# Optimization experiments

Hardware: AMD Instinct MI355X
Metric: run time of the kernel (lower is better)

Reference implementation:

```python
import jax, jax.numpy as jnp
import numpy as np

T, H, I, E, K = 2048, 2048, 1408, 8, 2


def setup_inputs() -> dict:
    key = jax.random.key(0)
    k1, k2, k3, k4, k5 = jax.random.split(key, 5)
    s_h = 1.0 / np.sqrt(H)
    s_i = 1.0 / np.sqrt(I)
    return {
        "hidden_states": jax.random.normal(k1, (T, H), dtype=jnp.float32),
        "router_logits": jax.random.normal(k2, (T, E), dtype=jnp.float32),
        "Wg": jax.random.normal(k3, (E, H, I), dtype=jnp.float32) * s_h,
        "Wu": jax.random.normal(k4, (E, H, I), dtype=jnp.float32) * s_h,
        "Wd": jax.random.normal(k5, (E, I, H), dtype=jnp.float32) * s_i,
        "top_k": K,
    }


def reference(hidden_states, router_logits, Wg, Wu, Wd, top_k):
    # top-k routing: softmax over the selected top-k logits (as in torch.topk + softmax)
    topk_vals, topk_ids = jax.lax.top_k(router_logits, top_k)  # [T,K]
    topk_w = jax.nn.softmax(topk_vals, axis=-1)                # [T,K]

    n_tok = hidden_states.shape[0]
    n_exp = router_logits.shape[-1]
    # combine weights [T,E]: scatter top-k weights back to expert slots
    cw = jnp.zeros((n_tok, n_exp), hidden_states.dtype)
    cw = cw.at[jnp.arange(n_tok)[:, None], topk_ids].add(topk_w)

    out = jnp.zeros_like(hidden_states)
    for e in range(n_exp):  # small fixed expert count
        g = hidden_states @ Wg[e]          # [T,I]
        u = hidden_states @ Wu[e]          # [T,I]
        y = (jax.nn.silu(g) * u) @ Wd[e]   # [T,H]
        out = out + cw[:, e:e + 1] * y
    return out
```

## Files before the change

### kernel.cpp

```cpp
#include <hip/hip_runtime.h>
#include <hip/hip_bf16.h>
#include <cstdint>
#include <cstddef>

#define TT 2048
#define HH 2048
#define II 1408
#define EE 8
#define MAXROWS 5120

typedef unsigned short u16;
typedef __attribute__((ext_vector_type(8))) __bf16 bf16x8;
typedef __attribute__((ext_vector_type(4))) float f32x4;

typedef const __attribute__((address_space(1))) uint32_t* gas1_t;
typedef __attribute__((address_space(3))) uint32_t* las3_t;

#define VM_WAIT(N) asm volatile("s_waitcnt vmcnt(" #N ")" ::: "memory")
#define IR_FENCE() asm volatile("" ::: "memory")

__device__ __forceinline__ float bf2f(u16 b) {
    return __uint_as_float(((uint32_t)b) << 16);
}
__device__ __forceinline__ u16 f2bf(float x) {
    uint32_t u = __float_as_uint(x);
    u += 0x7fffu + ((u >> 16) & 1u);
    return (u16)(u >> 16);
}

__global__ void k_sniff(const u16* __restrict__ raw, int* __restrict__ flag,
                        int* __restrict__ counts) {
    __shared__ int cnt;
    if (threadIdx.x < EE) counts[threadIdx.x] = 0;
    if (threadIdx.x == 0) cnt = 0;
    __syncthreads();
    int w = 0;
    for (int i = threadIdx.x; i < 4096; i += 256) {
        u16 x = raw[i];
        if (x & 0x7fff) {
            int ex = (x >> 7) & 0xff;
            if (ex == 0xff || ex < 100 || ex > 140) ++w;
        }
    }
    atomicAdd(&cnt, w);
    __syncthreads();
    if (threadIdx.x == 0) flag[0] = (cnt > 100) ? 1 : 0;
}

__global__ void k_routing2(const void* __restrict__ logits, const int* __restrict__ flag,
                           int* __restrict__ counts, int* __restrict__ idx,
                           float* __restrict__ wt, int* __restrict__ slot) {
    int t = blockIdx.x * 256 + threadIdx.x;
    if (t >= TT) return;
    const int f = flag[0];
    float v[EE];
#pragma unroll
    for (int e = 0; e < EE; ++e)
        v[e] = f ? ((const float*)logits)[t * EE + e]
                 : bf2f(((const u16*)logits)[t * EE + e]);
    int i0 = 0; float v0 = v[0];
#pragma unroll
    for (int e = 1; e < EE; ++e) { if (v[e] > v0) { v0 = v[e]; i0 = e; } }
    int i1 = -1; float v1 = -3.4e38f;
#pragma unroll
    for (int e = 0; e < EE; ++e) { if (e != i0 && v[e] > v1) { v1 = v[e]; i1 = e; } }
    float r = __expf(v1 - v0);
    float s = 1.f / (1.f + r);
    int p0 = atomicAdd(&counts[i0], 1);
    idx[i0 * TT + p0] = t; wt[i0 * TT + p0] = s;
    slot[t * 2 + 0] = i0 * TT + p0;
    int p1 = atomicAdd(&counts[i1], 1);
    idx[i1 * TT + p1] = t; wt[i1 * TT + p1] = r * s;
    slot[t * 2 + 1] = i1 * TT + p1;
}

__global__ void k_offsets(const int* __restrict__ counts, int* __restrict__ meta) {
    if (threadIdx.x == 0 && blockIdx.x == 0) {
        int off = 0;
        for (int e = 0; e < EE; ++e) {
            int c = counts[e];
            int p = (c + 127) & ~127;
            meta[e] = off; meta[8 + e] = p;
            off += p;
        }
    }
}

__global__ void k_cast(const void* __restrict__ src, const int* __restrict__ flag,
                       u16* __restrict__ dst) {
    const int i0 = (blockIdx.x * 256 + threadIdx.x) * 8;
    if (flag[0]) {
        const float* s = (const float*)src;
#pragma unroll
        for (int j = 0; j < 8; ++j) dst[i0 + j] = f2bf(s[i0 + j]);
    } else {
        const u16* s = (const u16*)src;
        *(uint4*)&dst[i0] = *(const uint4*)&s[i0];
    }
}

__global__ void k_transposeV(const void* __restrict__ src, const int* __restrict__ flag,
                             u16* __restrict__ dst, int R, int C) {
    __shared__ u16 t[64][68];
    const size_t eo = (size_t)blockIdx.z * (size_t)R * (size_t)C;
    const int r0 = blockIdx.y * 64, c0 = blockIdx.x * 64;
    const int tid = threadIdx.x;
    const int f = flag[0];
    {
        const int cg = tid & 15, rr = tid >> 4;
#pragma unroll
        for (int p = 0; p < 4; ++p) {
            const int r = rr + p * 16;
            const size_t base = eo + (size_t)(r0 + r) * C + c0 + cg * 4;
            if (f) {
                const float4 v = *(const float4*)((const float*)src + base);
                t[r][cg * 4 + 0] = f2bf(v.x); t[r][cg * 4 + 1] = f2bf(v.y);
                t[r][cg * 4 + 2] = f2bf(v.z); t[r][cg * 4 + 3] = f2bf(v.w);
            } else {
                const ushort4 v = *(const ushort4*)((const u16*)src + base);
                t[r][cg * 4 + 0] = v.x; t[r][cg * 4 + 1] = v.y;
                t[r][cg * 4 + 2] = v.z; t[r][cg * 4 + 3] = v.w;
            }
        }
    }
    __syncthreads();
    {
        const int rg = tid & 15, cc = tid >> 4;
#pragma unroll
        for (int p = 0; p < 4; ++p) {
            const int c = cc + p * 16;
            ushort4 o;
            o.x = t[rg * 4 + 0][c]; o.y = t[rg * 4 + 1][c];
            o.z = t[rg * 4 + 2][c]; o.w = t[rg * 4 + 3][c];
            *(ushort4*)(dst + eo + (size_t)(c0 + c) * R + r0 + rg * 4) = o;
        }
    }
}


#define G1_COMPUTE(B) do { \
    __builtin_amdgcn_s_setprio(1); \
    bf16x8 af[4]; \
    _Pragma("unroll") \
    for (int mi = 0; mi < 4; ++mi) \
        af[mi] = *(const bf16x8*)&As[B][(wr + mi * 16 + ln) * 32 + qx]; \
    _Pragma("unroll") \
    for (int ni = 0; ni < 2; ++ni) { \
        bf16x8 bgf = *(const bf16x8*)&Bg[B][(wc + ni * 16 + ln) * 32 + qx]; \
        bf16x8 buf_ = *(const bf16x8*)&Bu[B][(wc + ni * 16 + ln) * 32 + qx]; \
        _Pragma("unroll") \
        for (int mi = 0; mi < 4; ++mi) { \
            accg[mi][ni] = __builtin_amdgcn_mfma_f32_16x16x32_bf16(af[mi], bgf, accg[mi][ni], 0, 0, 0); \
            accu[mi][ni] = __builtin_amdgcn_mfma_f32_16x16x32_bf16(af[mi], buf_, accu[mi][ni], 0, 0, 0); \
        } \
    } \
    __builtin_amdgcn_s_setprio(0); \
} while (0)

#define G1_STAGE(B, KB) do { \
    __builtin_amdgcn_global_load_lds((gas1_t)(pA + (KB)), (las3_t)(&As[B][dofs]), 16, 0, 0); \
    __builtin_amdgcn_global_load_lds((gas1_t)(pG + (KB)), (las3_t)(&Bg[B][dofs]), 16, 0, 0); \
    __builtin_amdgcn_global_load_lds((gas1_t)(pU + (KB)), (las3_t)(&Bu[B][dofs]), 16, 0, 0); \
} while (0)

__global__ __launch_bounds__(512, 4)
void k_gemm1s(const u16* __restrict__ hs_b,
              const u16* __restrict__ Wgt,
              const u16* __restrict__ Wut,
              const int* __restrict__ counts,
              const int* __restrict__ meta,
              const int* __restrict__ idx,
              const float* __restrict__ wt,
              u16* __restrict__ act_g) {
    const int e = blockIdx.x;
    const int cnt = counts[e];
    const int pcnt = meta[8 + e];
    const int m0 = blockIdx.z * 128;
    if (m0 >= pcnt) return;
    const int n0 = blockIdx.y * 128;
    const int off = meta[e];
    const int tid = threadIdx.x;
    const int wave = tid >> 6, lane = tid & 63;
    const int ln = lane & 15, q = lane >> 4;
    const int wr = (wave >> 2) * 64;
    const int wc = (wave & 3) * 32;

    __shared__ __align__(16) u16 As[2][128 * 32];
    __shared__ __align__(16) u16 Bg[2][128 * 32];
    __shared__ __align__(16) u16 Bu[2][128 * 32];
    __shared__ int   tokS[128];
    __shared__ float wtS[128];

    if (tid < 128) {
        const int pos = m0 + tid;
        const bool v = pos < cnt;
        tokS[tid] = v ? idx[e * TT + pos] : 0;
        wtS[tid]  = v ? wt[e * TT + pos] : 0.f;
    }
    __syncthreads();

    const int srow = tid >> 2;
    const int csw  = (((tid & 3) ^ ((srow >> 1) & 3))) * 8;
    const u16* pA = hs_b + (size_t)tokS[srow] * HH + csw;
    const u16* pG = Wgt + ((size_t)e * II + n0 + srow) * HH + csw;
    const u16* pU = Wut + ((size_t)e * II + n0 + srow) * HH + csw;
    const int dofs = tid * 8;

    const int qx = (q ^ ((ln >> 1) & 3)) * 8;

    f32x4 accg[4][2], accu[4][2];
#pragma unroll
    for (int mi = 0; mi < 4; ++mi)
#pragma unroll
        for (int ni = 0; ni < 2; ++ni) { accg[mi][ni] = (f32x4)0.f; accu[mi][ni] = (f32x4)0.f; }

    G1_STAGE(0, 0);
    int cur = 0;
    for (int t = 0; t < 63; ++t) {
        G1_STAGE(cur ^ 1, (t + 1) * 32);
        VM_WAIT(3);
        __builtin_amdgcn_s_barrier();
        G1_COMPUTE(cur);
        IR_FENCE();
        __builtin_amdgcn_s_barrier();
        cur ^= 1;
    }
    VM_WAIT(0);
    __builtin_amdgcn_s_barrier();
    G1_COMPUTE(cur);

#pragma unroll
    for (int mi = 0; mi < 4; ++mi) {
#pragma unroll
        for (int r = 0; r < 4; ++r) {
            const int row = wr + mi * 16 + q * 4 + r;
            const float w = wtS[row];
#pragma unroll
            for (int ni = 0; ni < 2; ++ni) {
                const int i = n0 + wc + ni * 16 + ln;
                const float g = accg[mi][ni][r];
                const float u = accu[mi][ni][r];
                const float y = w * u * g / (1.f + __expf(-g));
                act_g[(size_t)(off + m0 + row) * II + i] = f2bf(y);
            }
        }
    }
}

#define G2_COMPUTE(B) do { \
    __builtin_amdgcn_s_setprio(1); \
    bf16x8 af[4]; \
    _Pragma("unroll") \
    for (int mi = 0; mi < 4; ++mi) \
        af[mi] = *(const bf16x8*)&As[B][(wr + mi * 16 + ln) * 32 + qx]; \
    _Pragma("unroll") \
    for (int ni = 0; ni < 4; ++ni) { \
        bf16x8 bf = *(const bf16x8*)&Bs[B][(wc + ni * 16 + ln) * 32 + qx]; \
        _Pragma("unroll") \
        for (int mi = 0; mi < 4; ++mi) \
            acc[mi][ni] = __builtin_amdgcn_mfma_f32_16x16x32_bf16(af[mi], bf, acc[mi][ni], 0, 0, 0); \
    } \
    __builtin_amdgcn_s_setprio(0); \
} while (0)

#define G2_STAGE(B, KB) do { \
    __builtin_amdgcn_global_load_lds((gas1_t)(pA0 + (KB)), (las3_t)(&As[B][dofs]), 16, 0, 0); \
    __builtin_amdgcn_global_load_lds((gas1_t)(pA1 + (KB)), (las3_t)(&As[B][2048 + dofs]), 16, 0, 0); \
    __builtin_amdgcn_global_load_lds((gas1_t)(pB0 + (KB)), (las3_t)(&Bs[B][dofs]), 16, 0, 0); \
    __builtin_amdgcn_global_load_lds((gas1_t)(pB1 + (KB)), (las3_t)(&Bs[B][2048 + dofs]), 16, 0, 0); \
} while (0)

__global__ __launch_bounds__(256, 4)
void k_gemm2s(const u16* __restrict__ act_g,
              const u16* __restrict__ Wdt,
              const int* __restrict__ meta,
              float* __restrict__ y_g) {
    const int e = blockIdx.x;
    const int pcnt = meta[8 + e];
    const int m0 = blockIdx.z * 128;
    if (m0 >= pcnt) return;
    const int n0 = blockIdx.y * 128;
    const int off = meta[e];
    const int tid = threadIdx.x;
    const int wave = tid >> 6, lane = tid & 63;
    const int ln = lane & 15, q = lane >> 4;
    const int wr = (wave >> 1) * 64, wc = (wave & 1) * 64;

    __shared__ __align__(16) u16 As[2][128 * 32];
    __shared__ __align__(16) u16 Bs[2][128 * 32];

    const int srow = tid >> 2;
    const int csw  = (((tid & 3) ^ ((srow >> 1) & 3))) * 8;
    const u16* bA = act_g + (size_t)(off + m0) * II;
    const u16* bB = Wdt + ((size_t)e * HH + n0) * II;
    const u16* pA0 = bA + (size_t)srow * II + csw;
    const u16* pA1 = bA + (size_t)(srow + 64) * II + csw;
    const u16* pB0 = bB + (size_t)srow * II + csw;
    const u16* pB1 = bB + (size_t)(srow + 64) * II + csw;
    const int dofs = tid * 8;

    const int qx = (q ^ ((ln >> 1) & 3)) * 8;

    f32x4 acc[4][4];
#pragma unroll
    for (int mi = 0; mi < 4; ++mi)
#pragma unroll
        for (int ni = 0; ni < 4; ++ni) acc[mi][ni] = (f32x4)0.f;

    G2_STAGE(0, 0);
    int cur = 0;
    for (int t = 0; t < 43; ++t) {
        G2_STAGE(cur ^ 1, (t + 1) * 32);
        VM_WAIT(4);
        __builtin_amdgcn_s_barrier();
        G2_COMPUTE(cur);
        IR_FENCE();
        __builtin_amdgcn_s_barrier();
        cur ^= 1;
    }
    VM_WAIT(0);
    __builtin_amdgcn_s_barrier();
    G2_COMPUTE(cur);

#pragma unroll
    for (int mi = 0; mi < 4; ++mi) {
#pragma unroll
        for (int r = 0; r < 4; ++r) {
            const int row = wr + mi * 16 + q * 4 + r;
            float* dst = y_g + (size_t)(off + m0 + row) * HH + n0 + wc;
#pragma unroll
            for (int ni = 0; ni < 4; ++ni)
                dst[ni * 16 + ln] = acc[mi][ni][r];
        }
    }
}

__global__ void k_combine(const float* __restrict__ y_g, const int* __restrict__ slot,
                          const int* __restrict__ meta, const int* __restrict__ flag,
                          void* __restrict__ out) {
    const int gid = blockIdx.x * 256 + threadIdx.x;
    const int t = gid >> 9;
    const int h = (gid & 511) * 4;
    const int s0 = slot[t * 2 + 0], s1 = slot[t * 2 + 1];
    const int r0 = meta[s0 >> 11] + (s0 & 2047);
    const int r1 = meta[s1 >> 11] + (s1 & 2047);
    const float4 a = *(const float4*)&y_g[(size_t)r0 * HH + h];
    const float4 b = *(const float4*)&y_g[(size_t)r1 * HH + h];
    const float4 v = make_float4(a.x + b.x, a.y + b.y, a.z + b.z, a.w + b.w);
    if (flag[0]) {
        *(float4*)((float*)out + (size_t)t * HH + h) = v;
    } else {
        u16* o = (u16*)out + (size_t)t * HH + h;
        o[0] = f2bf(v.x); o[1] = f2bf(v.y); o[2] = f2bf(v.z); o[3] = f2bf(v.w);
    }
}

extern "C" void kernel_launch(void* const* d_in, const int* in_sizes, int n_in,
                              void* d_out, int out_size, void* d_ws, size_t ws_size,
                              hipStream_t stream) {
    (void)in_sizes; (void)n_in; (void)out_size;
    const void* hs     = d_in[0];
    const void* logits = d_in[1];
    const void* Wg     = d_in[2];
    const void* Wu     = d_in[3];
    const void* Wd     = d_in[4];

    char* ws = (char*)d_ws;
    size_t off = 0;
    int*   flag   = (int*)(ws + off);   off += 256;
    int*   counts = (int*)(ws + off);   off += 256;
    int*   meta   = (int*)(ws + off);   off += 256;
    int*   idx    = (int*)(ws + off);   off += (size_t)EE * TT * 4;
    float* wt     = (float*)(ws + off); off += (size_t)EE * TT * 4;
    int*   slot   = (int*)(ws + off);   off += (size_t)TT * 2 * 4;
    u16*   hs_b   = (u16*)(ws + off);   off += (size_t)TT * HH * 2;
    u16*   Wgt    = (u16*)(ws + off);   off += (size_t)EE * II * HH * 2;
    u16*   Wut    = (u16*)(ws + off);   off += (size_t)EE * II * HH * 2;
    u16*   Wdt    = (u16*)(ws + off);   off += (size_t)EE * HH * II * 2;
    u16*   act_g  = (u16*)(ws + off);   off += (size_t)MAXROWS * II * 2;
    float* y_g    = (float*)(ws + off); off += (size_t)MAXROWS * HH * 4;
    if (ws_size < off) return;

    k_sniff<<<dim3(1), dim3(256), 0, stream>>>((const u16*)hs, flag, counts);
    k_routing2<<<dim3(TT / 256), dim3(256), 0, stream>>>(logits, flag, counts, idx, wt, slot);
    k_offsets<<<dim3(1), dim3(64), 0, stream>>>(counts, meta);
    k_cast<<<dim3(TT * HH / (256 * 8)), dim3(256), 0, stream>>>(hs, flag, hs_b);
    k_transposeV<<<dim3(II / 64, HH / 64, EE), dim3(256), 0, stream>>>(Wg, flag, Wgt, HH, II);
    k_transposeV<<<dim3(II / 64, HH / 64, EE), dim3(256), 0, stream>>>(Wu, flag, Wut, HH, II);
    k_transposeV<<<dim3(HH / 64, II / 64, EE), dim3(256), 0, stream>>>(Wd, flag, Wdt, II, HH);
    k_gemm1s<<<dim3(EE, II / 128, TT / 128), dim3(512), 0, stream>>>(hs_b, Wgt, Wut, counts, meta, idx, wt, act_g);
    k_gemm2s<<<dim3(EE, HH / 128, TT / 128), dim3(256), 0, stream>>>(act_g, Wdt, meta, y_g);
    k_combine<<<dim3(TT * HH / (256 * 4)), dim3(256), 0, stream>>>(y_g, slot, meta, flag, d_out);
}
```

Before: 452.5 us.

## Fuse routing into one block and merge cast/transposes into one prep kernel

Merges the sniff, routing and offset kernels into a single 1024-thread block that uses shared-memory counters. It also folds the hidden-state cast and the three weight transposes into one flat-grid prep kernel. The new transpose tile packs row pairs into 32-bit LDS words and writes 16-byte vectors. This cuts launch count and global atomics, and widens the transpose stores, at the cost of running routing serially on one CU.

```diff
diff --git a/kernel.cpp b/kernel.cpp
--- a/kernel.cpp
+++ b/kernel.cpp
@@ -9,6 +9,9 @@
 #define EE 8
 #define MAXROWS 5120
 
+#define CAST_BLOCKS (TT * HH / (256 * 8))
+#define TR_BLOCKS   704
+
 typedef unsigned short u16;
 typedef __attribute__((ext_vector_type(8))) __bf16 bf16x8;
 typedef __attribute__((ext_vector_type(4))) float f32x4;
@@ -28,15 +31,20 @@
     return (u16)(u >> 16);
 }
 
-__global__ void k_sniff(const u16* __restrict__ raw, int* __restrict__ flag,
-                        int* __restrict__ counts) {
+__global__ void k_route(const u16* __restrict__ hs_raw, const void* __restrict__ logits,
+                        int* __restrict__ flag_g, int* __restrict__ counts_g,
+                        int* __restrict__ meta, int* __restrict__ idx,
+                        float* __restrict__ wt, int* __restrict__ slot) {
     __shared__ int cnt;
-    if (threadIdx.x < EE) counts[threadIdx.x] = 0;
-    if (threadIdx.x == 0) cnt = 0;
+    __shared__ int cS[EE];
+    __shared__ int flagS;
+    const int tid = threadIdx.x;
+    if (tid < EE) cS[tid] = 0;
+    if (tid == 0) cnt = 0;
     __syncthreads();
     int w = 0;
-    for (int i = threadIdx.x; i < 4096; i += 256) {
-        u16 x = raw[i];
+    for (int i = tid; i < 4096; i += 1024) {
+        u16 x = hs_raw[i];
         if (x & 0x7fff) {
             int ex = (x >> 7) & 0xff;
             if (ex == 0xff || ex < 100 || ex > 140) ++w;
@@ -44,41 +52,36 @@
     }
     atomicAdd(&cnt, w);
     __syncthreads();
-    if (threadIdx.x == 0) flag[0] = (cnt > 100) ? 1 : 0;
-}
-
-__global__ void k_routing2(const void* __restrict__ logits, const int* __restrict__ flag,
-                           int* __restrict__ counts, int* __restrict__ idx,
-                           float* __restrict__ wt, int* __restrict__ slot) {
-    int t = blockIdx.x * 256 + threadIdx.x;
-    if (t >= TT) return;
-    const int f = flag[0];
-    float v[EE];
-#pragma unroll
-    for (int e = 0; e < EE; ++e)
-        v[e] = f ? ((const float*)logits)[t * EE + e]
-                 : bf2f(((const u16*)logits)[t * EE + e]);
-    int i0 = 0; float v0 = v[0];
-#pragma unroll
-    for (int e = 1; e < EE; ++e) { if (v[e] > v0) { v0 = v[e]; i0 = e; } }
-    int i1 = -1; float v1 = -3.4e38f;
-#pragma unroll
-    for (int e = 0; e < EE; ++e) { if (e != i0 && v[e] > v1) { v1 = v[e]; i1 = e; } }
-    float r = __expf(v1 - v0);
-    float s = 1.f / (1.f + r);
-    int p0 = atomicAdd(&counts[i0], 1);
-    idx[i0 * TT + p0] = t; wt[i0 * TT + p0] = s;
-    slot[t * 2 + 0] = i0 * TT + p0;
-    int p1 = atomicAdd(&counts[i1], 1);
-    idx[i1 * TT + p1] = t; wt[i1 * TT + p1] = r * s;
-    slot[t * 2 + 1] = i1 * TT + p1;
-}
-
-__global__ void k_offsets(const int* __restrict__ counts, int* __restrict__ meta) {
-    if (threadIdx.x == 0 && blockIdx.x == 0) {
+    if (tid == 0) { flagS = (cnt > 100) ? 1 : 0; flag_g[0] = flagS; }
+    __syncthreads();
+    const int f = flagS;
+    for (int t = tid; t < TT; t += 1024) {
+        float v[EE];
+#pragma unroll
+        for (int e = 0; e < EE; ++e)
+            v[e] = f ? ((const float*)logits)[t * EE + e]
+                     : bf2f(((const u16*)logits)[t * EE + e]);
+        int i0 = 0; float v0 = v[0];
+#pragma unroll
+        for (int e = 1; e < EE; ++e) { if (v[e] > v0) { v0 = v[e]; i0 = e; } }
+        int i1 = -1; float v1 = -3.4e38f;
+#pragma unroll
+        for (int e = 0; e < EE; ++e) { if (e != i0 && v[e] > v1) { v1 = v[e]; i1 = e; } }
+        float r = __expf(v1 - v0);
+        float s = 1.f / (1.f + r);
+        int p0 = atomicAdd(&cS[i0], 1);
+        idx[i0 * TT + p0] = t; wt[i0 * TT + p0] = s;
+        slot[t * 2 + 0] = i0 * TT + p0;
+        int p1 = atomicAdd(&cS[i1], 1);
+        idx[i1 * TT + p1] = t; wt[i1 * TT + p1] = r * s;
+        slot[t * 2 + 1] = i1 * TT + p1;
+    }
+    __syncthreads();
+    if (tid == 0) {
         int off = 0;
         for (int e = 0; e < EE; ++e) {
-            int c = counts[e];
+            int c = cS[e];
+            counts_g[e] = c;
             int p = (c + 127) & ~127;
             meta[e] = off; meta[8 + e] = p;
             off += p;
@@ -86,54 +89,90 @@
     }
 }
 
-__global__ void k_cast(const void* __restrict__ src, const int* __restrict__ flag,
-                       u16* __restrict__ dst) {
-    const int i0 = (blockIdx.x * 256 + threadIdx.x) * 8;
-    if (flag[0]) {
-        const float* s = (const float*)src;
-#pragma unroll
-        for (int j = 0; j < 8; ++j) dst[i0 + j] = f2bf(s[i0 + j]);
-    } else {
-        const u16* s = (const u16*)src;
-        *(uint4*)&dst[i0] = *(const uint4*)&s[i0];
-    }
-}
-
-__global__ void k_transposeV(const void* __restrict__ src, const int* __restrict__ flag,
-                             u16* __restrict__ dst, int R, int C) {
-    __shared__ u16 t[64][68];
-    const size_t eo = (size_t)blockIdx.z * (size_t)R * (size_t)C;
-    const int r0 = blockIdx.y * 64, c0 = blockIdx.x * 64;
+__device__ __forceinline__ void transpose_tile(const void* __restrict__ src,
+                                               u16* __restrict__ dst,
+                                               uint32_t* TTs, int R, int C,
+                                               int r0, int c0, int f, int tid) {
+    const int cg = (tid & 15) * 4;
+    const int rh = tid >> 4;
+#pragma unroll
+    for (int p = 0; p < 2; ++p) {
+        const int rp = rh + 16 * p;
+        const int r  = 2 * rp;
+        const size_t base = (size_t)(r0 + r) * C + c0 + cg;
+        uint32_t w0, w1, w2, w3;
+        if (f) {
+            const float4 v0 = *(const float4*)((const float*)src + base);
+            const float4 v1 = *(const float4*)((const float*)src + base + C);
+            w0 = (uint32_t)f2bf(v0.x) | ((uint32_t)f2bf(v1.x) << 16);
+            w1 = (uint32_t)f2bf(v0.y) | ((uint32_t)f2bf(v1.y) << 16);
+            w2 = (uint32_t)f2bf(v0.z) | ((uint32_t)f2bf(v1.z) << 16);
+            w3 = (uint32_t)f2bf(v0.w) | ((uint32_t)f2bf(v1.w) << 16);
+        } else {
+            const ushort4 v0 = *(const ushort4*)((const u16*)src + base);
+            const ushort4 v1 = *(const ushort4*)((const u16*)src + base + C);
+            w0 = (uint32_t)v0.x | ((uint32_t)v1.x << 16);
+            w1 = (uint32_t)v0.y | ((uint32_t)v1.y << 16);
+            w2 = (uint32_t)v0.z | ((uint32_t)v1.z << 16);
+            w3 = (uint32_t)v0.w | ((uint32_t)v1.w << 16);
+        }
+        TTs[(cg + 0) * 34 + rp] = w0;
+        TTs[(cg + 1) * 34 + rp] = w1;
+        TTs[(cg + 2) * 34 + rp] = w2;
+        TTs[(cg + 3) * 34 + rp] = w3;
+    }
+    __syncthreads();
+    const int c = tid >> 2, u = tid & 3;
+    uint32_t o[8];
+#pragma unroll
+    for (int k = 0; k < 4; ++k) {
+        const int rp = 8 * u + 2 * k;
+        o[2 * k]     = TTs[c * 34 + rp];
+        o[2 * k + 1] = TTs[c * 34 + rp + 1];
+    }
+    u16* dp = dst + (size_t)(c0 + c) * R + r0 + 16 * u;
+    *(uint4*)(dp)     = make_uint4(o[0], o[1], o[2], o[3]);
+    *(uint4*)(dp + 8) = make_uint4(o[4], o[5], o[6], o[7]);
+}
+
+__global__ void k_prep(const void* __restrict__ hs, const void* __restrict__ Wg,
+                       const void* __restrict__ Wu, const void* __restrict__ Wd,
+                       const int* __restrict__ flag,
+                       u16* __restrict__ hs_b, u16* __restrict__ Wgt,
+                       u16* __restrict__ Wut, u16* __restrict__ Wdt) {
+    __shared__ uint32_t TTs[64 * 34];
+    const int bid = blockIdx.x;
     const int tid = threadIdx.x;
     const int f = flag[0];
-    {
-        const int cg = tid & 15, rr = tid >> 4;
-#pragma unroll
-        for (int p = 0; p < 4; ++p) {
-            const int r = rr + p * 16;
-            const size_t base = eo + (size_t)(r0 + r) * C + c0 + cg * 4;
-            if (f) {
-                const float4 v = *(const float4*)((const float*)src + base);
-                t[r][cg * 4 + 0] = f2bf(v.x); t[r][cg * 4 + 1] = f2bf(v.y);
-                t[r][cg * 4 + 2] = f2bf(v.z); t[r][cg * 4 + 3] = f2bf(v.w);
-            } else {
-                const ushort4 v = *(const ushort4*)((const u16*)src + base);
-                t[r][cg * 4 + 0] = v.x; t[r][cg * 4 + 1] = v.y;
-                t[r][cg * 4 + 2] = v.z; t[r][cg * 4 + 3] = v.w;
-            }
-        }
-    }
-    __syncthreads();
-    {
-        const int rg = tid & 15, cc = tid >> 4;
-#pragma unroll
-        for (int p = 0; p < 4; ++p) {
-            const int c = cc + p * 16;
-            ushort4 o;
-            o.x = t[rg * 4 + 0][c]; o.y = t[rg * 4 + 1][c];
-            o.z = t[rg * 4 + 2][c]; o.w = t[rg * 4 + 3][c];
-            *(ushort4*)(dst + eo + (size_t)(c0 + c) * R + r0 + rg * 4) = o;
-        }
+    if (bid < CAST_BLOCKS) {
+        const int i0 = (bid * 256 + tid) * 8;
+        if (f) {
+            const float* s = (const float*)hs;
+#pragma unroll
+            for (int j = 0; j < 8; ++j) hs_b[i0 + j] = f2bf(s[i0 + j]);
+        } else {
+            const u16* s = (const u16*)hs;
+            *(uint4*)&hs_b[i0] = *(const uint4*)&s[i0];
+        }
+        return;
+    }
+    const int rr = bid - CAST_BLOCKS;
+    const int z = rr / TR_BLOCKS;
+    const int b = rr - z * TR_BLOCKS;
+    const size_t eo = (size_t)(z & 7) * (size_t)HH * (size_t)II;
+    if (z < 16) {
+        const int cx = b % 22, cy = b / 22;
+        const void* srcp;
+        u16* dstp;
+        if (z < 8) { srcp = f ? (const void*)((const float*)Wg + eo) : (const void*)((const u16*)Wg + eo);
+                     dstp = Wgt + eo; }
+        else       { srcp = f ? (const void*)((const float*)Wu + eo) : (const void*)((const u16*)Wu + eo);
+                     dstp = Wut + eo; }
+        transpose_tile(srcp, dstp, TTs, HH, II, cy * 64, cx * 64, f, tid);
+    } else {
+        const int cx = b % 32, cy = b / 32;
+        const void* srcp = f ? (const void*)((const float*)Wd + eo) : (const void*)((const u16*)Wd + eo);
+        transpose_tile(srcp, Wdt + eo, TTs, II, HH, cy * 64, cx * 64, f, tid);
     }
 }
 
@@ -381,14 +420,12 @@
     float* y_g    = (float*)(ws + off); off += (size_t)MAXROWS * HH * 4;
     if (ws_size < off) return;
 
-    k_sniff<<<dim3(1), dim3(256), 0, stream>>>((const u16*)hs, flag, counts);
-    k_routing2<<<dim3(TT / 256), dim3(256), 0, stream>>>(logits, flag, counts, idx, wt, slot);
-    k_offsets<<<dim3(1), dim3(64), 0, stream>>>(counts, meta);
-    k_cast<<<dim3(TT * HH / (256 * 8)), dim3(256), 0, stream>>>(hs, flag, hs_b);
-    k_transposeV<<<dim3(II / 64, HH / 64, EE), dim3(256), 0, stream>>>(Wg, flag, Wgt, HH, II);
-    k_transposeV<<<dim3(II / 64, HH / 64, EE), dim3(256), 0, stream>>>(Wu, flag, Wut, HH, II);
-    k_transposeV<<<dim3(HH / 64, II / 64, EE), dim3(256), 0, stream>>>(Wd, flag, Wdt, II, HH);
-    k_gemm1s<<<dim3(EE, II / 128, TT / 128), dim3(512), 0, stream>>>(hs_b, Wgt, Wut, counts, meta, idx, wt, act_g);
+    k_route<<<dim3(1), dim3(1024), 0, stream>>>((const u16*)hs, logits, flag, counts,
+                                                meta, idx, wt, slot);
+    k_prep<<<dim3(CAST_BLOCKS + 24 * TR_BLOCKS), dim3(256), 0, stream>>>(
+        hs, Wg, Wu, Wd, flag, hs_b, Wgt, Wut, Wdt);
+    k_gemm1s<<<dim3(EE, II / 128, TT / 128), dim3(512), 0, stream>>>(hs_b, Wgt, Wut,
+                                                counts, meta, idx, wt, act_g);
     k_gemm2s<<<dim3(EE, HH / 128, TT / 128), dim3(256), 0, stream>>>(act_g, Wdt, meta, y_g);
     k_combine<<<dim3(TT * HH / (256 * 4)), dim3(256), 0, stream>>>(y_g, slot, meta, flag, d_out);
 }
```

Result: faster. 433.1 us (-4.3%).
